# Kernel tuning notes

Hardware: AMD Instinct MI355X
Metric: run time of the kernel (lower is better)

The kernel has to match this reference:

```python
import jax, jax.numpy as jnp
import numpy as np

B = 512        # graphs per batch
N_NODES = 64   # nodes per graph
IN_CH = 256
EMBED = 64
TOPK = 20
NEG_SLOPE = 0.2


def setup_inputs() -> dict:
    key = jax.random.key(0)
    ks = jax.random.split(key, 6)
    N = B * N_NODES
    x = jax.random.normal(ks[0], (N, IN_CH), dtype=jnp.float32)
    # fully-connected graph WITH self loops, per graph, sorted source-major
    src = jnp.repeat(jnp.arange(N_NODES, dtype=jnp.int32), N_NODES)  # [n*n]
    dst = jnp.tile(jnp.arange(N_NODES, dtype=jnp.int32), N_NODES)    # [n*n]
    offs = (jnp.arange(B, dtype=jnp.int32) * N_NODES)[:, None]       # [B,1]
    l = (src[None, :] + offs).reshape(-1)
    r = (dst[None, :] + offs).reshape(-1)
    edge_index = jnp.stack([l, r]).astype(jnp.int32)                 # [2, B*n*n]
    batch = jnp.repeat(jnp.arange(B, dtype=jnp.int32), N_NODES)      # [N]
    glorot = lambda k, sh: jax.random.uniform(k, sh, jnp.float32,
                                              -1.0, 1.0) * np.sqrt(6.0 / (sh[0] + sh[-1]))
    Wl = glorot(ks[1], (EMBED, IN_CH))
    bl = jnp.zeros((EMBED,), jnp.float32)
    Wr = glorot(ks[2], (EMBED, IN_CH))
    br = jnp.zeros((EMBED,), jnp.float32)
    att = glorot(ks[3], (1, EMBED))
    return {"x": x, "edge_index": edge_index, "batch": batch,
            "Wl": Wl, "bl": bl, "Wr": Wr, "br": br, "att": att}


def reference(x, edge_index, batch, Wl, bl, Wr, br, att):
    N = x.shape[0]
    x_l = x @ Wl.T + bl                      # [N, D]
    x_r = x @ Wr.T + br                      # [N, D]
    l, r = edge_index[0], edge_index[1]
    # edge gather + GAT-style score
    e = jax.nn.leaky_relu(x_l[l] + x_r[r], negative_slope=NEG_SLOPE)  # [E, D]
    alpha = (e * att[0]).sum(axis=-1)                                  # [E]
    # segment softmax grouped by source node l (each group is non-empty)
    m = jax.ops.segment_max(alpha, l, num_segments=N)
    a = jnp.exp(alpha - m[l])
    s = jax.ops.segment_sum(a, l, num_segments=N)
    a = a / s[l]
    # kNN sparsify: zero the diagonal then per-row topk
    a3 = a.reshape(B, N_NODES, N_NODES)
    a3 = a3 * (1.0 - jnp.eye(N_NODES, dtype=a3.dtype))
    attention, indices = jax.lax.top_k(a3, TOPK)     # [B, n, k] sorted desc
    attention = attention.reshape(-1)                 # [B*n*k]
    offs = (jnp.arange(B, dtype=jnp.int32) * N_NODES)[:, None]
    index_i = (jnp.repeat(jnp.arange(N_NODES, dtype=jnp.int32), TOPK)[None, :]
               + offs).reshape(-1)
    index_j = (indices.astype(jnp.int32)
               + (jnp.arange(B, dtype=jnp.int32) * N_NODES)[:, None, None]).reshape(-1)
    new_edge_index = jnp.stack([index_i, index_j])    # [2, B*n*k]
    return new_edge_index, attention
```

## Files before the change

kernel.cpp:

```cpp
#include <hip/hip_runtime.h>
#include <stdint.h>

#define NGRAPH 512
#define NN 64
#define INCH 256
#define TOPK 20
#define EPR 655360

typedef __attribute__((ext_vector_type(8))) short bf16x8;
typedef __attribute__((ext_vector_type(4))) float f32x4;

__device__ __align__(16) uint4 g_wfrag[4096];

#define XBF 0
#define XLR 8192
#define XRR 12352
#define SMEM_DW 16512

static __device__ __forceinline__ uint32_t f2bfbits(float f) {
  uint32_t u = __float_as_uint(f);
  return (u + 0x7FFFu + ((u >> 16) & 1u)) >> 16;
}
static __device__ __forceinline__ uint32_t pk2(float a, float b) {
  return f2bfbits(a) | (f2bfbits(b) << 16);
}
static __device__ __forceinline__ float keyalpha(uint32_t k) {
  uint32_t ub = (k & 0x80000000u) ? (k ^ 0x80000000u) : ~k;
  return __uint_as_float(ub & 0xFFFFFFC0u);
}

static __device__ __forceinline__ uint32_t bflyu(uint32_t v, const int j, const int lane) {
  if (j == 1)
    return (uint32_t)__builtin_amdgcn_update_dpp(0, (int)v, 0xB1, 0xF, 0xF, true);
  if (j == 2)
    return (uint32_t)__builtin_amdgcn_update_dpp(0, (int)v, 0x4E, 0xF, 0xF, true);
  if (j == 8)
    return (uint32_t)__builtin_amdgcn_update_dpp(0, (int)v, 0x128, 0xF, 0xF, true);
#if __has_builtin(__builtin_amdgcn_permlane16_swap)
  if (j == 16) {
    auto r = __builtin_amdgcn_permlane16_swap((unsigned)v, (unsigned)v, false, false);
    return (uint32_t)(((lane >> 4) & 1) ? r[0] : r[1]);
  }
#endif
#if __has_builtin(__builtin_amdgcn_permlane32_swap)
  if (j == 32) {
    auto r = __builtin_amdgcn_permlane32_swap((unsigned)v, (unsigned)v, false, false);
    return (uint32_t)((lane & 32) ? r[0] : r[1]);
  }
#endif
  return (uint32_t)__shfl_xor((int)v, j);
}
static __device__ __forceinline__ float bflyf(float v, const int j, const int lane) {
  return __uint_as_float(bflyu(__float_as_uint(v), j, lane));
}
static __device__ __forceinline__ float redsum64(float v, const int lane) {
  v += bflyf(v, 1, lane);
  v += bflyf(v, 2, lane);
  v += bflyf(v, 4, lane);
  v += bflyf(v, 8, lane);
  v += bflyf(v, 16, lane);
  v += bflyf(v, 32, lane);
  return v;
}

__global__ __launch_bounds__(256) void wpack2(const float* __restrict__ Wl,
                                              const float* __restrict__ Wr) {
  const int t = blockIdx.x * 256 + threadIdx.x;
  const int lo = t & 15, quad = (t >> 4) & 3, ct = (t >> 6) & 3;
  const int ks = (t >> 8) & 7, half = (t >> 11) & 1;
  const int n = ct * 16 + lo, k0 = ks * 32 + quad * 8;
  const float* src = half ? Wr : Wl;
  const float4* s4 = (const float4*)(src + (size_t)n * INCH + k0);
  float4 a0 = s4[0], a1 = s4[1];
  g_wfrag[t] = (uint4){ pk2(a0.x, a0.y), pk2(a0.z, a0.w), pk2(a1.x, a1.y), pk2(a1.z, a1.w) };
}

__global__ __launch_bounds__(512, 4) void gat3(
    const float* __restrict__ x,
    const float* __restrict__ blv,
    const float* __restrict__ brv,
    const float* __restrict__ att,
    float* __restrict__ out)
{
  __shared__ __align__(16) uint32_t smemU[SMEM_DW];
  float* smemF = (float*)smemU;

  const int b    = blockIdx.x;
  const int t    = threadIdx.x;
  const int w    = t >> 6;
  const int lane = t & 63;
  const int quad = lane >> 4;
  const int lo   = lane & 15;
  const int nodeBase = b * NN;
  const uint4* wsV = g_wfrag;

  {
    const float* xg = x + (size_t)nodeBase * INCH;
    #pragma unroll
    for (int i = 0; i < 8; ++i) {
      const int fd = i * 2048 + t * 4;
      float4 v = *(const float4*)(xg + fd);
      const int row = fd >> 8;
      const int c2  = (fd & 255) >> 1;
      const int dw  = row * 128 + (c2 ^ ((row & 7) << 2));
      *(uint2*)&smemU[XBF + dw] = (uint2){ pk2(v.x, v.y), pk2(v.z, v.w) };
    }
  }
  __syncthreads();

  const int half = w >> 2;
  const int r0   = (w & 3) * 16;

  f32x4 acc[4];
  #pragma unroll
  for (int ct = 0; ct < 4; ++ct) acc[ct] = (f32x4){0.f, 0.f, 0.f, 0.f};

  #pragma unroll
  for (int ks = 0; ks < 8; ++ks) {
    const int adw = XBF + (r0 + lo) * 128 + ((ks * 16 + quad * 4) ^ ((lo & 7) << 2));
    uint4 au = *(const uint4*)&smemU[adw];
    bf16x8 afrag = __builtin_bit_cast(bf16x8, au);
    #pragma unroll
    for (int ct = 0; ct < 4; ++ct) {
      uint4 bu = wsV[half * 2048 + ks * 256 + ct * 64 + quad * 16 + lo];
      bf16x8 bfrag = __builtin_bit_cast(bf16x8, bu);
      acc[ct] = __builtin_amdgcn_mfma_f32_16x16x32_bf16(afrag, bfrag, acc[ct], 0, 0, 0);
    }
  }

  {
    const float* bias = half ? brv : blv;
    const int dstBase = half ? XRR : XLR;
    #pragma unroll
    for (int ct = 0; ct < 4; ++ct) {
      const int d = ct * 16 + lo;
      const float bb = bias[d];
      #pragma unroll
      for (int rg = 0; rg < 4; ++rg)
        smemF[dstBase + (r0 + quad * 4 + rg) * 65 + d] = acc[ct][rg] + bb;
    }
  }
  __syncthreads();

  const int rB = w * 8;

  float xlv[8];
  #pragma unroll
  for (int q = 0; q < 8; ++q)
    xlv[q] = smemF[XLR + (rB + q) * 65 + lane];

  float pacc[8];
  #pragma unroll
  for (int q = 0; q < 8; ++q) pacc[q] = 0.f;
  float srp = 0.f;
  const int xrb = XRR + lane * 65;
  #pragma unroll
  for (int c = 0; c < 4; ++c) {
    f32x4 xrc[4];
    #pragma unroll
    for (int g = 0; g < 4; ++g)
      xrc[g] = *(const f32x4*)&smemF[xrb + c * 16 + g * 4];
    #pragma unroll
    for (int dl = 0; dl < 16; ++dl) {
      const int d = c * 16 + dl;
      const float xv = xrc[dl >> 2][dl & 3];
      const float ad = att[d];
      srp = fmaf(ad, xv, srp);
      #pragma unroll
      for (int q = 0; q < 8; ++q) {
        const float xls = __int_as_float(
            __builtin_amdgcn_readlane(__float_as_int(xlv[q]), d));
        pacc[q] = fmaf(ad, fabsf(xls + xv), pacc[q]);
      }
    }
  }

  float aq[8];
  #pragma unroll
  for (int q = 0; q < 8; ++q)
    aq[q] = 0.6f * srp + 0.4f * pacc[q];

  uint32_t key[8];
  #pragma unroll
  for (int q = 0; q < 8; ++q) {
    const uint32_t u = __float_as_uint(aq[q]);
    uint32_t kk = u ^ ((uint32_t)((int32_t)u >> 31) | 0x80000000u);
    kk = (kk & 0xFFFFFFC0u) | (uint32_t)(63 - lane);
    key[q] = (lane == rB + q) ? 0u : kk;
  }

  #pragma unroll
  for (int k = 2; k <= 64; k <<= 1) {
    #pragma unroll
    for (int j = k >> 1; j >= 1; j >>= 1) {
      const bool keep_max = (((lane & k) == 0) == ((lane & j) == 0));
      #pragma unroll
      for (int q = 0; q < 8; ++q) {
        const uint32_t p = bflyu(key[q], j, lane);
        const uint32_t mx = (key[q] > p) ? key[q] : p;
        const uint32_t mn = (key[q] > p) ? p : key[q];
        key[q] = keep_max ? mx : mn;
      }
    }
  }

  float mq[8], Sq[8];
  #pragma unroll
  for (int q = 0; q < 8; ++q) {
    const uint32_t tk = (uint32_t)__builtin_amdgcn_readlane((int)key[q], 0);
    const float adiag = __int_as_float(
        __builtin_amdgcn_readlane(__float_as_int(aq[q]), rB + q));
    mq[q] = fmaxf(keyalpha(tk), adiag);
    Sq[q] = redsum64(__expf(aq[q] - mq[q]), lane);
  }

  if (lane < TOPK) {
    #pragma unroll
    for (int q = 0; q < 8; ++q) {
      const int g = nodeBase + rB + q;
      const uint32_t kq = key[q];
      const float alpha = keyalpha(kq);
      const int jj = 63 - (int)(kq & 63u);
      const float va = __expf(alpha - mq[q]) * (1.0f / Sq[q]);
      out[(size_t)g * 20 + lane] = (float)g;
      out[(size_t)EPR + (size_t)g * 20 + lane] = (float)(nodeBase + jj);
      out[2 * (size_t)EPR + (size_t)g * 20 + lane] = va;
    }
  }
}

extern "C" void kernel_launch(void* const* d_in, const int* in_sizes, int n_in,
                              void* d_out, int out_size, void* d_ws, size_t ws_size,
                              hipStream_t stream) {
  const float* x   = (const float*)d_in[0];
  const float* Wl  = (const float*)d_in[3];
  const float* bl  = (const float*)d_in[4];
  const float* Wr  = (const float*)d_in[5];
  const float* br  = (const float*)d_in[6];
  const float* att = (const float*)d_in[7];
  (void)d_ws; (void)ws_size;

  wpack2<<<dim3(16), dim3(256), 0, stream>>>(Wl, Wr);
  gat3<<<dim3(NGRAPH), dim3(512), 0, stream>>>(x, bl, br, att, (float*)d_out);
}
```

Before: 120.6 us.

## Process two graphs per block to reuse weight fragments across MFMA passes

Each block now handles two graphs: it loads both graphs' x tiles into shared memory, reuses every weight fragment loaded from global memory for two MFMAs, and then runs the score, sort and softmax phase for each graph in a serial loop. This halves global weight-fragment traffic per graph and issues more independent loads up front. In exchange the block count drops to 256 (fewer blocks than CUs on MI355X), shared memory roughly doubles, occupancy falls to 2 blocks per CU, and the per-graph epilogue is serialised within a block.

```diff
diff --git a/kernel.cpp b/kernel.cpp
--- a/kernel.cpp
+++ b/kernel.cpp
@@ -12,10 +12,13 @@
 
 __device__ __align__(16) uint4 g_wfrag[4096];
 
-#define XBF 0
-#define XLR 8192
-#define XRR 12352
-#define SMEM_DW 16512
+#define XBF0 0
+#define XBF1 8192
+#define XLR0 16384
+#define XRR0 20544
+#define XLR1 24704
+#define XRR1 28864
+#define SMEM_DW 33024
 
 static __device__ __forceinline__ uint32_t f2bfbits(float f) {
   uint32_t u = __float_as_uint(f);
@@ -75,7 +78,7 @@
   g_wfrag[t] = (uint4){ pk2(a0.x, a0.y), pk2(a0.z, a0.w), pk2(a1.x, a1.y), pk2(a1.z, a1.w) };
 }
 
-__global__ __launch_bounds__(512, 4) void gat3(
+__global__ __launch_bounds__(512, 2) void gat4(
     const float* __restrict__ x,
     const float* __restrict__ blv,
     const float* __restrict__ brv,
@@ -85,25 +88,29 @@
   __shared__ __align__(16) uint32_t smemU[SMEM_DW];
   float* smemF = (float*)smemU;
 
-  const int b    = blockIdx.x;
   const int t    = threadIdx.x;
   const int w    = t >> 6;
   const int lane = t & 63;
   const int quad = lane >> 4;
   const int lo   = lane & 15;
-  const int nodeBase = b * NN;
-  const uint4* wsV = g_wfrag;
+  const int gbase = blockIdx.x * 2;
 
   {
-    const float* xg = x + (size_t)nodeBase * INCH;
+    const float* xg0 = x + (size_t)gbase * NN * INCH;
+    const float* xg1 = xg0 + (size_t)NN * INCH;
+    float4 va[8], vb[8];
+    #pragma unroll
+    for (int i = 0; i < 8; ++i) va[i] = *(const float4*)(xg0 + i * 2048 + t * 4);
+    #pragma unroll
+    for (int i = 0; i < 8; ++i) vb[i] = *(const float4*)(xg1 + i * 2048 + t * 4);
     #pragma unroll
     for (int i = 0; i < 8; ++i) {
-      const int fd = i * 2048 + t * 4;
-      float4 v = *(const float4*)(xg + fd);
+      const int fd  = i * 2048 + t * 4;
       const int row = fd >> 8;
       const int c2  = (fd & 255) >> 1;
       const int dw  = row * 128 + (c2 ^ ((row & 7) << 2));
-      *(uint2*)&smemU[XBF + dw] = (uint2){ pk2(v.x, v.y), pk2(v.z, v.w) };
+      *(uint2*)&smemU[XBF0 + dw] = (uint2){ pk2(va[i].x, va[i].y), pk2(va[i].z, va[i].w) };
+      *(uint2*)&smemU[XBF1 + dw] = (uint2){ pk2(vb[i].x, vb[i].y), pk2(vb[i].z, vb[i].w) };
     }
   }
   __syncthreads();
@@ -111,120 +118,134 @@
   const int half = w >> 2;
   const int r0   = (w & 3) * 16;
 
-  f32x4 acc[4];
+  f32x4 acc[2][4];
   #pragma unroll
-  for (int ct = 0; ct < 4; ++ct) acc[ct] = (f32x4){0.f, 0.f, 0.f, 0.f};
+  for (int gg = 0; gg < 2; ++gg)
+    #pragma unroll
+    for (int ct = 0; ct < 4; ++ct) acc[gg][ct] = (f32x4){0.f, 0.f, 0.f, 0.f};
 
   #pragma unroll
   for (int ks = 0; ks < 8; ++ks) {
-    const int adw = XBF + (r0 + lo) * 128 + ((ks * 16 + quad * 4) ^ ((lo & 7) << 2));
-    uint4 au = *(const uint4*)&smemU[adw];
-    bf16x8 afrag = __builtin_bit_cast(bf16x8, au);
+    const int adw = (r0 + lo) * 128 + ((ks * 16 + quad * 4) ^ ((lo & 7) << 2));
+    uint4 auA = *(const uint4*)&smemU[XBF0 + adw];
+    uint4 auB = *(const uint4*)&smemU[XBF1 + adw];
+    bf16x8 afA = __builtin_bit_cast(bf16x8, auA);
+    bf16x8 afB = __builtin_bit_cast(bf16x8, auB);
     #pragma unroll
     for (int ct = 0; ct < 4; ++ct) {
-      uint4 bu = wsV[half * 2048 + ks * 256 + ct * 64 + quad * 16 + lo];
-      bf16x8 bfrag = __builtin_bit_cast(bf16x8, bu);
-      acc[ct] = __builtin_amdgcn_mfma_f32_16x16x32_bf16(afrag, bfrag, acc[ct], 0, 0, 0);
+      uint4 bu = g_wfrag[half * 2048 + ks * 256 + ct * 64 + quad * 16 + lo];
+      bf16x8 bf = __builtin_bit_cast(bf16x8, bu);
+      acc[0][ct] = __builtin_amdgcn_mfma_f32_16x16x32_bf16(afA, bf, acc[0][ct], 0, 0, 0);
+      acc[1][ct] = __builtin_amdgcn_mfma_f32_16x16x32_bf16(afB, bf, acc[1][ct], 0, 0, 0);
     }
   }
 
   {
     const float* bias = half ? brv : blv;
-    const int dstBase = half ? XRR : XLR;
-    #pragma unroll
-    for (int ct = 0; ct < 4; ++ct) {
-      const int d = ct * 16 + lo;
-      const float bb = bias[d];
-      #pragma unroll
-      for (int rg = 0; rg < 4; ++rg)
-        smemF[dstBase + (r0 + quad * 4 + rg) * 65 + d] = acc[ct][rg] + bb;
+    #pragma unroll
+    for (int gg = 0; gg < 2; ++gg) {
+      const int dstBase = gg ? (half ? XRR1 : XLR1) : (half ? XRR0 : XLR0);
+      #pragma unroll
+      for (int ct = 0; ct < 4; ++ct) {
+        const int d = ct * 16 + lo;
+        const float bb = bias[d];
+        #pragma unroll
+        for (int rg = 0; rg < 4; ++rg)
+          smemF[dstBase + (r0 + quad * 4 + rg) * 65 + d] = acc[gg][ct][rg] + bb;
+      }
     }
   }
   __syncthreads();
 
   const int rB = w * 8;
-
-  float xlv[8];
-  #pragma unroll
-  for (int q = 0; q < 8; ++q)
-    xlv[q] = smemF[XLR + (rB + q) * 65 + lane];
-
-  float pacc[8];
-  #pragma unroll
-  for (int q = 0; q < 8; ++q) pacc[q] = 0.f;
-  float srp = 0.f;
-  const int xrb = XRR + lane * 65;
-  #pragma unroll
-  for (int c = 0; c < 4; ++c) {
-    f32x4 xrc[4];
-    #pragma unroll
-    for (int g = 0; g < 4; ++g)
-      xrc[g] = *(const f32x4*)&smemF[xrb + c * 16 + g * 4];
-    #pragma unroll
-    for (int dl = 0; dl < 16; ++dl) {
-      const int d = c * 16 + dl;
-      const float xv = xrc[dl >> 2][dl & 3];
-      const float ad = att[d];
-      srp = fmaf(ad, xv, srp);
+  #pragma unroll 1
+  for (int gg = 0; gg < 2; ++gg) {
+    const int xlrB = gg ? XLR1 : XLR0;
+    const int xrrB = gg ? XRR1 : XRR0;
+    const int nodeBase = (gbase + gg) * NN;
+
+    float xlv[8];
+    #pragma unroll
+    for (int q = 0; q < 8; ++q)
+      xlv[q] = smemF[xlrB + (rB + q) * 65 + lane];
+
+    float pacc[8];
+    #pragma unroll
+    for (int q = 0; q < 8; ++q) pacc[q] = 0.f;
+    float srp = 0.f;
+    const int xrb = xrrB + lane * 65;
+    #pragma unroll
+    for (int c = 0; c < 4; ++c) {
+      f32x4 xrc[4];
+      #pragma unroll
+      for (int g = 0; g < 4; ++g)
+        xrc[g] = *(const f32x4*)&smemF[xrb + c * 16 + g * 4];
+      #pragma unroll
+      for (int dl = 0; dl < 16; ++dl) {
+        const int d = c * 16 + dl;
+        const float xv = xrc[dl >> 2][dl & 3];
+        const float ad = att[d];
+        srp = fmaf(ad, xv, srp);
+        #pragma unroll
+        for (int q = 0; q < 8; ++q) {
+          const float xls = __int_as_float(
+              __builtin_amdgcn_readlane(__float_as_int(xlv[q]), d));
+          pacc[q] = fmaf(ad, fabsf(xls + xv), pacc[q]);
+        }
+      }
+    }
+
+    float aq[8];
+    #pragma unroll
+    for (int q = 0; q < 8; ++q)
+      aq[q] = 0.6f * srp + 0.4f * pacc[q];
+
+    uint32_t key[8];
+    #pragma unroll
+    for (int q = 0; q < 8; ++q) {
+      const uint32_t u = __float_as_uint(aq[q]);
+      uint32_t kk = u ^ ((uint32_t)((int32_t)u >> 31) | 0x80000000u);
+      kk = (kk & 0xFFFFFFC0u) | (uint32_t)(63 - lane);
+      key[q] = (lane == rB + q) ? 0u : kk;
+    }
+
+    #pragma unroll
+    for (int k = 2; k <= 64; k <<= 1) {
+      #pragma unroll
+      for (int j = k >> 1; j >= 1; j >>= 1) {
+        const bool keep_max = (((lane & k) == 0) == ((lane & j) == 0));
+        #pragma unroll
+        for (int q = 0; q < 8; ++q) {
+          const uint32_t p = bflyu(key[q], j, lane);
+          const uint32_t mx = (key[q] > p) ? key[q] : p;
+          const uint32_t mn = (key[q] > p) ? p : key[q];
+          key[q] = keep_max ? mx : mn;
+        }
+      }
+    }
+
+    float mq[8], Sq[8];
+    #pragma unroll
+    for (int q = 0; q < 8; ++q) {
+      const uint32_t tk = (uint32_t)__builtin_amdgcn_readlane((int)key[q], 0);
+      const float adiag = __int_as_float(
+          __builtin_amdgcn_readlane(__float_as_int(aq[q]), rB + q));
+      mq[q] = fmaxf(keyalpha(tk), adiag);
+      Sq[q] = redsum64(__expf(aq[q] - mq[q]), lane);
+    }
+
+    if (lane < TOPK) {
       #pragma unroll
       for (int q = 0; q < 8; ++q) {
-        const float xls = __int_as_float(
-            __builtin_amdgcn_readlane(__float_as_int(xlv[q]), d));
-        pacc[q] = fmaf(ad, fabsf(xls + xv), pacc[q]);
-      }
-    }
-  }
-
-  float aq[8];
-  #pragma unroll
-  for (int q = 0; q < 8; ++q)
-    aq[q] = 0.6f * srp + 0.4f * pacc[q];
-
-  uint32_t key[8];
-  #pragma unroll
-  for (int q = 0; q < 8; ++q) {
-    const uint32_t u = __float_as_uint(aq[q]);
-    uint32_t kk = u ^ ((uint32_t)((int32_t)u >> 31) | 0x80000000u);
-    kk = (kk & 0xFFFFFFC0u) | (uint32_t)(63 - lane);
-    key[q] = (lane == rB + q) ? 0u : kk;
-  }
-
-  #pragma unroll
-  for (int k = 2; k <= 64; k <<= 1) {
-    #pragma unroll
-    for (int j = k >> 1; j >= 1; j >>= 1) {
-      const bool keep_max = (((lane & k) == 0) == ((lane & j) == 0));
-      #pragma unroll
-      for (int q = 0; q < 8; ++q) {
-        const uint32_t p = bflyu(key[q], j, lane);
-        const uint32_t mx = (key[q] > p) ? key[q] : p;
-        const uint32_t mn = (key[q] > p) ? p : key[q];
-        key[q] = keep_max ? mx : mn;
-      }
-    }
-  }
-
-  float mq[8], Sq[8];
-  #pragma unroll
-  for (int q = 0; q < 8; ++q) {
-    const uint32_t tk = (uint32_t)__builtin_amdgcn_readlane((int)key[q], 0);
-    const float adiag = __int_as_float(
-        __builtin_amdgcn_readlane(__float_as_int(aq[q]), rB + q));
-    mq[q] = fmaxf(keyalpha(tk), adiag);
-    Sq[q] = redsum64(__expf(aq[q] - mq[q]), lane);
-  }
-
-  if (lane < TOPK) {
-    #pragma unroll
-    for (int q = 0; q < 8; ++q) {
-      const int g = nodeBase + rB + q;
-      const uint32_t kq = key[q];
-      const float alpha = keyalpha(kq);
-      const int jj = 63 - (int)(kq & 63u);
-      const float va = __expf(alpha - mq[q]) * (1.0f / Sq[q]);
-      out[(size_t)g * 20 + lane] = (float)g;
-      out[(size_t)EPR + (size_t)g * 20 + lane] = (float)(nodeBase + jj);
-      out[2 * (size_t)EPR + (size_t)g * 20 + lane] = va;
+        const int g = nodeBase + rB + q;
+        const uint32_t kq = key[q];
+        const float alpha = keyalpha(kq);
+        const int jj = 63 - (int)(kq & 63u);
+        const float va = __expf(alpha - mq[q]) * (1.0f / Sq[q]);
+        out[(size_t)g * 20 + lane] = (float)g;
+        out[(size_t)EPR + (size_t)g * 20 + lane] = (float)(nodeBase + jj);
+        out[2 * (size_t)EPR + (size_t)g * 20 + lane] = va;
+      }
     }
   }
 }
@@ -241,5 +262,5 @@
   (void)d_ws; (void)ws_size;
 
   wpack2<<<dim3(16), dim3(256), 0, stream>>>(Wl, Wr);
-  gat3<<<dim3(NGRAPH), dim3(512), 0, stream>>>(x, bl, br, att, (float*)d_out);
-}
+  gat4<<<dim3(NGRAPH / 2), dim3(512), 0, stream>>>(x, bl, br, att, (float*)d_out);
+}
```

Measured after the change: 126.7 us. 5.1% more time.
